# Kernel tuning notes

Hardware: AMD Instinct MI355X
Metric: run time of the kernel (lower is better)

Reference implementation:

```python
import jax, jax.numpy as jnp
import numpy as np

N = 6000      # nodes
E = 150000    # edges (avg degree ~25, close to _AVG_DEGREE=23.4)
K = 9         # (lmax+1)^2 spherical coefficients, lmax=2
C = 128       # sphere_channels
H = 8         # num_heads
V = 16        # attn_value_channels (H*V == C)
L = 2         # num_layers
B = 512       # num_distance_basis
RMAX = 5.0
EPS = 1e-6


def _rms_sh(x):
    # rms_norm_sh-style normalization over (coefficients, channels)
    return x * jax.lax.rsqrt(jnp.mean(x * x, axis=(-2, -1), keepdims=True) + EPS)


def _seg_softmax(logits, seg, n):
    # numerically-stable per-destination-node softmax over incoming edges
    m = jax.ops.segment_max(logits, seg, num_segments=n)
    ex = jnp.exp(logits - m[seg])
    s = jax.ops.segment_sum(ex, seg, num_segments=n)
    return ex / (s[seg] + 1e-9)


def setup_inputs() -> dict:
    key = jax.random.key(0)
    ks = jax.random.split(key, 24)
    s = 0.02
    inp = {
        # graph / features
        "atom_feats": jax.random.randint(ks[0], (N, 4), 0, 10),
        "bond_feats": jax.random.randint(ks[1], (E, 3), 0, 8),
        "edge_index": jax.random.randint(ks[2], (2, E), 0, N),
        "edge_distance": jax.random.uniform(ks[3], (E,), jnp.float32, 0.0, RMAX),
        # embeddings
        "atom_emb": jax.random.normal(ks[4], (4, 10, C), jnp.float32) * s,
        "bond_emb": jax.random.normal(ks[5], (3, 8, C), jnp.float32) * s,
        # distance-basis edge MLP (edge_channels_list = [512, 128, 128])
        "W_rbf1": jax.random.normal(ks[6], (B, C), jnp.float32) * s,
        "b_rbf1": jnp.zeros((C,), jnp.float32),
        "W_rbf2": jax.random.normal(ks[7], (C, C), jnp.float32) * s,
        "b_rbf2": jnp.zeros((C,), jnp.float32),
        # per-layer attention params (stacked over L)
        "Wa1": jax.random.normal(ks[8], (L, 3 * C, C), jnp.float32) * s,
        "Wa2": jax.random.normal(ks[9], (L, C, H), jnp.float32) * s,
        "Wv": jax.random.normal(ks[10], (L, C, H * V), jnp.float32) * s,
        "Wg": jax.random.normal(ks[11], (L, C, H), jnp.float32) * s,
        "Wo": jax.random.normal(ks[12], (L, H * V, C), jnp.float32) * s,
        # per-layer FFN params
        "Wf1": jax.random.normal(ks[13], (L, C, 512), jnp.float32) * s,
        "Wf2": jax.random.normal(ks[14], (L, 512, C), jnp.float32) * s,
    }
    return inp


def _forward(atom_feats, bond_feats, edge_index, edge_distance,
             atom_emb, bond_emb, W_rbf1, b_rbf1, W_rbf2, b_rbf2,
             Wa1, Wa2, Wv, Wg, Wo, Wf1, Wf2):
    src, dst = edge_index[0], edge_index[1]

    # --- atom embedding into l=0 coefficient of the SH node state ---
    a0 = sum(atom_emb[f][atom_feats[:, f]] for f in range(4))      # [N, C]
    x = jnp.zeros((N, K, C), a0.dtype).at[:, 0, :].set(a0)          # [N, K, C]

    # --- gaussian distance basis + edge embedding MLP + bond features ---
    centers = jnp.linspace(0.0, RMAX, B)
    width = RMAX / B
    rbf = jnp.exp(-((edge_distance[:, None] - centers[None, :]) / width) ** 2)  # [E, B]
    e = jax.nn.silu(rbf @ W_rbf1 + b_rbf1) @ W_rbf2 + b_rbf2                    # [E, C]
    e = e + sum(bond_emb[f][bond_feats[:, f]] for f in range(3))

    for l in range(L):
        # ---- SO(2)-style graph attention block ----
        xn = _rms_sh(x)
        xs = xn[src]                                                 # [E, K, C] gather
        inv = jnp.concatenate([xn[src, 0], xn[dst, 0], e], axis=-1)  # invariant feats [E, 3C]
        logits = jax.nn.silu(inv @ Wa1[l]) @ Wa2[l]                  # [E, H]
        alpha = _seg_softmax(logits, dst, N)                         # renormalized attention
        gate = jax.nn.sigmoid(e @ Wg[l])                             # edge-embedding gate [E, H]
        v = jnp.einsum('ekc,chv->ekhv', xs, Wv[l].reshape(C, H, V))  # [E, K, H, V]
        v = v * (alpha * gate)[:, None, :, None]
        msg = v.reshape(E, K, H * V)
        agg = jax.ops.segment_sum(msg, dst, num_segments=N)          # scatter [N, K, H*V]
        x = x + jnp.einsum('nkd,dc->nkc', agg, Wo[l])

        # ---- equivariant FFN with separable S2-style activation ----
        xn = _rms_sh(x)
        h = jnp.einsum('nkc,cf->nkf', xn, Wf1[l])                    # [N, K, 512]
        h0 = jax.nn.silu(h[:, :1, :])                                # l=0 scalar path
        hr = h[:, 1:, :] * jax.nn.sigmoid(h[:, :1, :])               # gated l>0 path
        h = jnp.concatenate([h0, hr], axis=1)
        x = x + jnp.einsum('nkf,fc->nkc', h, Wf2[l])

    return _rms_sh(x)


def reference(atom_feats, bond_feats, edge_index, edge_distance,
              atom_emb, bond_emb, W_rbf1, b_rbf1, W_rbf2, b_rbf2,
              Wa1, Wa2, Wv, Wg, Wo, Wf1, Wf2):
    return _forward(atom_feats, bond_feats, edge_index, edge_distance,
                    atom_emb, bond_emb, W_rbf1, b_rbf1, W_rbf2, b_rbf2,
                    Wa1, Wa2, Wv, Wg, Wo, Wf1, Wf2)
```

## Files before the change

kernel.cpp:

```cpp
#include <hip/hip_runtime.h>

#define NN 6000
#define NE 150000
#define TBM 2048
#define TROWS (TBM + 1)

typedef unsigned int uint;
typedef unsigned short ushort;
typedef __attribute__((ext_vector_type(8))) short short8v;
typedef __attribute__((ext_vector_type(4))) float float4v;

__device__ __forceinline__ float siluf(float x) { return x / (1.f + __expf(-x)); }
__device__ __forceinline__ float sigmf(float x) { return 1.f / (1.f + __expf(-x)); }
__device__ __forceinline__ uint pack2bf(float lo, float hi) {
    uint ul = __float_as_uint(lo);
    ul = (ul + 0x7fffu + ((ul >> 16) & 1u)) >> 16;
    uint uh = __float_as_uint(hi);
    uh = ((uh + 0x7fffu + ((uh >> 16) & 1u)) >> 16) << 16;
    return ul | uh;
}
__device__ __forceinline__ ushort f2bf(float f) {
    uint u = __float_as_uint(f);
    return (ushort)((u + 0x7fffu + ((u >> 16) & 1u)) >> 16);
}
__device__ __forceinline__ float2 up2(uint u) {
    return make_float2(__uint_as_float(u << 16), __uint_as_float(u & 0xffff0000u));
}

__global__ __launch_bounds__(256)
void k_prep(const float* __restrict__ W2, const float* __restrict__ b2,
            const float* __restrict__ Wa1, const float* __restrict__ Wg,
            const float* __restrict__ bemb,
            const float* __restrict__ Wf1, const float* __restrict__ Wf2,
            const float* __restrict__ Wv, const float* __restrict__ Wa2,
            const float* __restrict__ Wo,
            float* __restrict__ W2A, float* __restrict__ W2G,
            float* __restrict__ bA, float* __restrict__ bG,
            uint* __restrict__ BAcb, float* __restrict__ BGc,
            ushort* __restrict__ Wf1x, ushort* __restrict__ Wf2x,
            ushort* __restrict__ Wvx, ushort* __restrict__ Wa1sx,
            ushort* __restrict__ Wa1dx, ushort* __restrict__ Wa2x,
            ushort* __restrict__ Wox)
{
    __shared__ float w2_s[8][132];
    const int l = blockIdx.y, bx = blockIdx.x, tid = threadIdx.x;
    const float* Wa1e = Wa1 + (size_t)l * 384 * 128 + 256 * 128;
    const float* Wgl  = Wg  + (size_t)l * 128 * 8;

    if (bx < 16) {
        const int i0 = bx * 8;
        for (int q = tid; q < 8 * 32; q += 256) {
            int ni = q >> 5, j4 = (q & 31) * 4;
            *reinterpret_cast<float4*>(&w2_s[ni][j4]) =
                *reinterpret_cast<const float4*>(&W2[(size_t)(i0 + ni) * 128 + j4]);
        }
        __syncthreads();
        const int j = tid & 127, ng = tid >> 7;
        float a[4] = {0.f, 0.f, 0.f, 0.f};
        #pragma unroll 4
        for (int k4 = 0; k4 < 128; k4 += 4) {
            float w0 = Wa1e[(k4 + 0) * 128 + j];
            float w1 = Wa1e[(k4 + 1) * 128 + j];
            float w2v = Wa1e[(k4 + 2) * 128 + j];
            float w3 = Wa1e[(k4 + 3) * 128 + j];
            #pragma unroll
            for (int r = 0; r < 4; ++r) {
                const float4 xv = *reinterpret_cast<const float4*>(&w2_s[ng * 4 + r][k4]);
                a[r] += xv.x * w0 + xv.y * w1 + xv.z * w2v + xv.w * w3;
            }
        }
        #pragma unroll
        for (int r = 0; r < 4; ++r)
            W2A[(size_t)l * 16384 + (size_t)(i0 + ng * 4 + r) * 128 + j] = a[r];
    } else if (bx == 16) {
        const int i = tid & 127, hq = tid >> 7;
        float a[4] = {0.f, 0.f, 0.f, 0.f};
        for (int k = 0; k < 128; ++k) {
            float w = W2[(size_t)i * 128 + k];
            const float4 g4 = *reinterpret_cast<const float4*>(&Wgl[k * 8 + hq * 4]);
            a[0] += w * g4.x; a[1] += w * g4.y; a[2] += w * g4.z; a[3] += w * g4.w;
        }
        #pragma unroll
        for (int q = 0; q < 4; ++q)
            W2G[(size_t)l * 1024 + (size_t)i * 8 + hq * 4 + q] = a[q];
    } else if (bx == 17) {
        if (tid < 128) {
            float s = 0.f;
            for (int k = 0; k < 128; ++k) s += b2[k] * Wa1e[k * 128 + tid];
            bA[l * 128 + tid] = s;
        } else if (tid < 136) {
            int h = tid - 128;
            float s = 0.f;
            for (int k = 0; k < 128; ++k) s += b2[k] * Wgl[k * 8 + h];
            bG[l * 8 + h] = s;
        }
    } else if (bx < 274) {
        const int cb = (bx - 18) * 2 + (tid >> 7);
        const int c = tid & 127;
        const int b[3] = {cb >> 6, (cb >> 3) & 7, cb & 7};
        float s = 0.f;
        #pragma unroll
        for (int f = 0; f < 3; ++f) {
            const float* er = &bemb[(size_t)(f * 8 + b[f]) * 128];
            for (int k = 0; k < 128; ++k)
                s += er[k] * Wa1e[k * 128 + c];
        }
        float hi = __shfl_down(s, 1, 64);
        if ((c & 1) == 0)
            BAcb[(size_t)l * 512 * 64 + (size_t)cb * 64 + (c >> 1)] = pack2bf(s, hi);
        if (c < 8) {
            float g = 0.f;
            #pragma unroll
            for (int f = 0; f < 3; ++f) {
                const float* er = &bemb[(size_t)(f * 8 + b[f]) * 128];
                for (int k = 0; k < 128; ++k)
                    g += er[k] * Wgl[k * 8 + c];
            }
            BGc[(size_t)l * 512 * 8 + (size_t)cb * 8 + c] = g;
        }
    } else {
        const int sub = (bx - 274) * 4 + (tid >> 6);
        const int lane = tid & 63;
        if (sub < 128) {
            const int nt = sub >> 2, kt = sub & 3;
            const float* src = Wf1 + (size_t)l * 65536;
            ushort* dst = Wf1x + (size_t)l * 65536 + ((size_t)sub * 64 + lane) * 8;
            #pragma unroll
            for (int j = 0; j < 8; ++j)
                dst[j] = f2bf(src[(size_t)(kt * 32 + (lane >> 4) * 8 + j) * 512 + nt * 16 + (lane & 15)]);
        } else if (sub < 256) {
            const int b2x = sub - 128;
            const int nt = b2x >> 4, kt = b2x & 15;
            const float* src = Wf2 + (size_t)l * 65536;
            ushort* dst = Wf2x + (size_t)l * 65536 + ((size_t)b2x * 64 + lane) * 8;
            #pragma unroll
            for (int j = 0; j < 8; ++j)
                dst[j] = f2bf(src[(size_t)(kt * 32 + (lane >> 4) * 8 + j) * 128 + nt * 16 + (lane & 15)]);
        } else if (sub < 352) {
            const int b3 = sub - 256;
            const int mat = b3 >> 5, blk = b3 & 31;
            const int nt = blk >> 2, kt = blk & 3;
            const float* src;
            ushort* dst;
            if (mat == 0)      { src = Wv  + (size_t)l * 16384;             dst = Wvx   + (size_t)l * 16384; }
            else if (mat == 1) { src = Wa1 + (size_t)l * 384 * 128;         dst = Wa1sx + (size_t)l * 16384; }
            else               { src = Wa1 + (size_t)l * 384 * 128 + 16384; dst = Wa1dx + (size_t)l * 16384; }
            dst += ((size_t)blk * 64 + lane) * 8;
            #pragma unroll
            for (int j = 0; j < 8; ++j)
                dst[j] = f2bf(src[(size_t)(kt * 32 + (lane >> 4) * 8 + j) * 128 + nt * 16 + (lane & 15)]);
        } else if (sub < 356) {
            const int kt = sub - 352;
            const int col = lane & 15;
            const float* src = Wa2 + (size_t)l * 128 * 8;
            ushort* dst = Wa2x + (size_t)l * 2048 + ((size_t)kt * 64 + lane) * 8;
            #pragma unroll
            for (int j = 0; j < 8; ++j) {
                int krow = kt * 32 + (lane >> 4) * 8 + j;
                dst[j] = (col < 8) ? f2bf(src[(size_t)krow * 8 + col]) : (ushort)0;
            }
        } else {
            const int blk = sub - 356;
            const int nt = blk >> 2, kt = blk & 3;
            const float* src = Wo + (size_t)l * 16384;
            ushort* dst = Wox + (size_t)l * 16384 + ((size_t)blk * 64 + lane) * 8;
            #pragma unroll
            for (int j = 0; j < 8; ++j)
                dst[j] = f2bf(src[(size_t)(kt * 32 + (lane >> 4) * 8 + j) * 128 + nt * 16 + (lane & 15)]);
        }
    }
}

__device__ __forceinline__
void node_gemm3(const ushort a_s[16][136], int tid, int n0,
                const ushort* __restrict__ Wvx, const ushort* __restrict__ Wa1sx,
                const ushort* __restrict__ Wa1dx,
                uint* __restrict__ Vb, uint* __restrict__ Psb, uint* __restrict__ Pdb)
{
    const int l = tid & 63, wq = tid >> 6;
    const int lr = l & 15, lk = l >> 4;
    #pragma unroll
    for (int jb = 0; jb < 6; ++jb) {
        int job = wq * 6 + jb;
        int mat = job >> 3, nt = job & 7;
        const ushort* W = (mat == 0) ? Wvx : (mat == 1 ? Wa1sx : Wa1dx);
        uint* O = (mat == 0) ? Vb : (mat == 1 ? Psb : Pdb);
        float4v acc = (float4v){0.f, 0.f, 0.f, 0.f};
        #pragma unroll
        for (int ks = 0; ks < 4; ++ks) {
            short8v af = *reinterpret_cast<const short8v*>(&a_s[lr][lk * 8 + ks * 32]);
            short8v bf = *reinterpret_cast<const short8v*>(&W[((size_t)(nt * 4 + ks) * 64 + l) * 8]);
            acc = __builtin_amdgcn_mfma_f32_16x16x32_bf16(af, bf, acc, 0, 0, 0);
        }
        #pragma unroll
        for (int r = 0; r < 4; ++r) {
            float v = acc[r];
            float vn = __shfl_xor(v, 1, 64);
            if ((l & 1) == 0) {
                int row = lk * 4 + r, col = nt * 16 + lr;
                O[(size_t)(n0 + row) * 64 + (col >> 1)] = pack2bf(v, vn);
            }
        }
    }
}

__device__ __forceinline__
void node_gemm3_8w(const ushort a_s[16][136], int tid, int n0,
                   const ushort* __restrict__ Wvx, const ushort* __restrict__ Wa1sx,
                   const ushort* __restrict__ Wa1dx,
                   uint* __restrict__ Vb, uint* __restrict__ Psb, uint* __restrict__ Pdb)
{
    const int l = tid & 63, w = tid >> 6;
    const int lr = l & 15, lk = l >> 4;
    #pragma unroll
    for (int jb = 0; jb < 3; ++jb) {
        int job = w * 3 + jb;
        int mat = job >> 3, nt = job & 7;
        const ushort* W = (mat == 0) ? Wvx : (mat == 1 ? Wa1sx : Wa1dx);
        uint* O = (mat == 0) ? Vb : (mat == 1 ? Psb : Pdb);
        float4v acc = (float4v){0.f, 0.f, 0.f, 0.f};
        #pragma unroll
        for (int ks = 0; ks < 4; ++ks) {
            short8v af = *reinterpret_cast<const short8v*>(&a_s[lr][lk * 8 + ks * 32]);
            short8v bf = *reinterpret_cast<const short8v*>(&W[((size_t)(nt * 4 + ks) * 64 + l) * 8]);
            acc = __builtin_amdgcn_mfma_f32_16x16x32_bf16(af, bf, acc, 0, 0, 0);
        }
        #pragma unroll
        for (int r = 0; r < 4; ++r) {
            float v = acc[r];
            float vn = __shfl_xor(v, 1, 64);
            if ((l & 1) == 0) {
                int row = lk * 4 + r, col = nt * 16 + lr;
                O[(size_t)(n0 + row) * 64 + (col >> 1)] = pack2bf(v, vn);
            }
        }
    }
}

__global__ __launch_bounds__(256)
void k_prep2(const float* __restrict__ W1, const float* __restrict__ b1,
             const float* __restrict__ W2A, const float* __restrict__ W2G,
             const float* __restrict__ bA, const float* __restrict__ bG,
             uint* __restrict__ TAb, float* __restrict__ TG,
             const int* __restrict__ af, const float* __restrict__ aemb,
             float* __restrict__ x, int* __restrict__ deg,
             const ushort* __restrict__ Wvx, const ushort* __restrict__ Wa1sx,
             const ushort* __restrict__ Wa1dx,
             uint* __restrict__ Vb, uint* __restrict__ Psb, uint* __restrict__ Pdb)
{
    __shared__ float rbf_s[8][32];
    __shared__ int   bs_s[8];
    __shared__ float t1_s[8][132];
    __shared__ ushort a_s[16][136];
    const int tid = threadIdx.x, bx = blockIdx.x;

    if (bx < 514) {
        const int l = (bx >= 257) ? 1 : 0;
        const int r0 = (bx - l * 257) * 8;
        {
            int ri = tid >> 5, j = tid & 31;
            int row = min(r0 + ri, TBM);
            float d = (float)row * (5.0f / TBM);
            const float step = 5.0f / 511.0f;
            const float invw = 512.0f / 5.0f;
            int b0 = (int)(d * (511.0f / 5.0f) + 0.5f);
            int bs = min(max(b0 - 16, 0), 512 - 32);
            if (j == 0) bs_s[ri] = bs;
            float z = (d - (float)(bs + j) * step) * invw;
            rbf_s[ri][j] = __expf(-z * z);
        }
        __syncthreads();
        #pragma unroll
        for (int pass = 0; pass < 4; ++pass) {
            int idx = pass * 256 + tid;
            int ri = idx >> 7, c = idx & 127;
            int bs = bs_s[ri];
            float t = b1[c];
            #pragma unroll
            for (int j = 0; j < 32; ++j)
                t += rbf_s[ri][j] * W1[(bs + j) * 128 + c];
            t1_s[ri][c] = siluf(t);
        }
        __syncthreads();

        const float* W2Al = W2A + (size_t)l * 16384;
        const int c = tid & 127, ng = tid >> 7;
        float a[4];
        #pragma unroll
        for (int r = 0; r < 4; ++r) a[r] = bA[l * 128 + c];
        #pragma unroll 4
        for (int k4 = 0; k4 < 128; k4 += 4) {
            float w0 = W2Al[(k4 + 0) * 128 + c];
            float w1 = W2Al[(k4 + 1) * 128 + c];
            float w2v = W2Al[(k4 + 2) * 128 + c];
            float w3 = W2Al[(k4 + 3) * 128 + c];
            #pragma unroll
            for (int r = 0; r < 4; ++r) {
                const float4 xv = *reinterpret_cast<const float4*>(&t1_s[ng * 4 + r][k4]);
                a[r] += xv.x * w0 + xv.y * w1 + xv.z * w2v + xv.w * w3;
            }
        }
        #pragma unroll
        for (int r = 0; r < 4; ++r) {
            float hi = __shfl_down(a[r], 1, 64);
            int row = r0 + ng * 4 + r;
            if (((c & 1) == 0) && row <= TBM)
                TAb[(size_t)l * TROWS * 64 + (size_t)row * 64 + (c >> 1)] = pack2bf(a[r], hi);
        }
        if (tid < 64) {
            int ri = tid >> 3, h = tid & 7;
            int row = r0 + ri;
            if (row <= TBM) {
                const float* W2Gl = W2G + (size_t)l * 1024;
                float s = bG[l * 8 + h];
                #pragma unroll 8
                for (int k = 0; k < 128; ++k)
                    s += t1_s[ri][k] * W2Gl[k * 8 + h];
                TG[(size_t)l * TROWS * 8 + (size_t)row * 8 + h] = s;
            }
        }
    } else {
        const int n0 = (bx - 514) * 16;
        if (tid < 16) deg[n0 + tid] = 0;
        {
            int ni = tid >> 4, c8 = (tid & 15) * 8;
            int n = n0 + ni;
            float v[8];
            #pragma unroll
            for (int q = 0; q < 8; ++q) v[q] = 0.f;
            #pragma unroll
            for (int f = 0; f < 4; ++f) {
                int idx = af[n * 4 + f];
                const float* er = &aemb[(size_t)(f * 10 + idx) * 128 + c8];
                float4 e0 = *reinterpret_cast<const float4*>(er);
                float4 e1 = *reinterpret_cast<const float4*>(er + 4);
                v[0] += e0.x; v[1] += e0.y; v[2] += e0.z; v[3] += e0.w;
                v[4] += e1.x; v[5] += e1.y; v[6] += e1.z; v[7] += e1.w;
            }
            float* xr = &x[(size_t)n * 128 + c8];
            *reinterpret_cast<float4*>(xr)     = make_float4(v[0], v[1], v[2], v[3]);
            *reinterpret_cast<float4*>(xr + 4) = make_float4(v[4], v[5], v[6], v[7]);
            float ss = 0.f;
            #pragma unroll
            for (int q = 0; q < 8; ++q) ss += v[q] * v[q];
            #pragma unroll
            for (int m = 1; m < 16; m <<= 1) ss += __shfl_xor(ss, m, 16);
            float r = rsqrtf(ss * (1.0f / 1152.0f) + 1e-6f);
            uint4 pk;
            pk.x = pack2bf(v[0] * r, v[1] * r);
            pk.y = pack2bf(v[2] * r, v[3] * r);
            pk.z = pack2bf(v[4] * r, v[5] * r);
            pk.w = pack2bf(v[6] * r, v[7] * r);
            *reinterpret_cast<uint4*>(&a_s[ni][c8]) = pk;
        }
        __syncthreads();
        node_gemm3(a_s, tid, n0, Wvx, Wa1sx, Wa1dx, Vb, Psb, Pdb);
    }
}

__global__ __launch_bounds__(256)
void k_hist(const int* __restrict__ eidx, int* __restrict__ deg)
{
    int e = blockIdx.x * 256 + threadIdx.x;
    if (e < NE) atomicAdd(&deg[eidx[NE + e]], 1);
}

__global__ __launch_bounds__(1024)
void k_scan(const int* __restrict__ deg, int* __restrict__ off, int* __restrict__ cursor)
{
    __shared__ int part[1024];
    const int t = threadIdx.x;
    const int base = t * 6;
    int loc[6]; int s = 0;
    #pragma unroll
    for (int i = 0; i < 6; ++i) {
        int d = (base + i < NN) ? deg[base + i] : 0;
        loc[i] = s; s += d;
    }
    part[t] = s;
    __syncthreads();
    for (int o = 1; o < 1024; o <<= 1) {
        int v = (t >= o) ? part[t - o] : 0;
        __syncthreads();
        part[t] += v;
        __syncthreads();
    }
    int pre = (t > 0) ? part[t - 1] : 0;
    #pragma unroll
    for (int i = 0; i < 6; ++i) {
        if (base + i < NN) {
            int v = pre + loc[i];
            off[base + i] = v;
            cursor[base + i] = v;
        }
    }
    if (t == 1023) off[NN] = part[1023];
}

__global__ __launch_bounds__(256)
void k_fill(const int* __restrict__ eidx, const int* __restrict__ bondf,
            const float* __restrict__ dist, int* __restrict__ cursor,
            int* __restrict__ srcp, int4* __restrict__ erec)
{
    int e = blockIdx.x * 256 + threadIdx.x;
    if (e < NE) {
        int d = eidx[NE + e];
        int p = atomicAdd(&cursor[d], 1);
        int sn = eidx[e];
        srcp[p] = sn;
        erec[p] = make_int4(sn, d, __float_as_int(dist[e]),
                            bondf[e * 3 + 0] * 64 + bondf[e * 3 + 1] * 8 + bondf[e * 3 + 2]);
    }
}

__global__ __launch_bounds__(256)
void k_attn(const int4* __restrict__ erec,
            const uint* __restrict__ Psb, const uint* __restrict__ Pdb,
            const uint* __restrict__ TAbl, const float* __restrict__ TGl,
            const uint* __restrict__ BAcbl, const float* __restrict__ BGcl,
            const ushort* __restrict__ Wa2xl,
            float2* __restrict__ nex)
{
    __shared__ ushort t_s[32][136];
    __shared__ float gate_s[32][8];
    const int tid = threadIdx.x;
    const int p0 = blockIdx.x * 32;

    {
        const int ei = tid >> 3, g = tid & 7;
        const int p = min(p0 + ei, NE - 1);
        const int4 er = erec[p];
        const int sn = er.x, dn = er.y;
        const float d = __int_as_float(er.z);
        const int cb = er.w;
        float u = d * ((float)TBM / 5.0f);
        int i = min((int)u, TBM - 1);
        float f = u - (float)i, f1 = 1.f - f;

        uint ps[8], pd[8], t0[8], t1v[8], ba[8];
        {
            const uint4* pp = reinterpret_cast<const uint4*>(&Psb[(size_t)sn * 64 + g * 8]);
            uint4 a = pp[0], b = pp[1];
            ps[0]=a.x; ps[1]=a.y; ps[2]=a.z; ps[3]=a.w; ps[4]=b.x; ps[5]=b.y; ps[6]=b.z; ps[7]=b.w;
            pp = reinterpret_cast<const uint4*>(&Pdb[(size_t)dn * 64 + g * 8]);
            a = pp[0]; b = pp[1];
            pd[0]=a.x; pd[1]=a.y; pd[2]=a.z; pd[3]=a.w; pd[4]=b.x; pd[5]=b.y; pd[6]=b.z; pd[7]=b.w;
            pp = reinterpret_cast<const uint4*>(&TAbl[(size_t)i * 64 + g * 8]);
            a = pp[0]; b = pp[1];
            t0[0]=a.x; t0[1]=a.y; t0[2]=a.z; t0[3]=a.w; t0[4]=b.x; t0[5]=b.y; t0[6]=b.z; t0[7]=b.w;
            pp = reinterpret_cast<const uint4*>(&TAbl[(size_t)(i + 1) * 64 + g * 8]);
            a = pp[0]; b = pp[1];
            t1v[0]=a.x; t1v[1]=a.y; t1v[2]=a.z; t1v[3]=a.w; t1v[4]=b.x; t1v[5]=b.y; t1v[6]=b.z; t1v[7]=b.w;
            pp = reinterpret_cast<const uint4*>(&BAcbl[(size_t)cb * 64 + g * 8]);
            a = pp[0]; b = pp[1];
            ba[0]=a.x; ba[1]=a.y; ba[2]=a.z; ba[3]=a.w; ba[4]=b.x; ba[5]=b.y; ba[6]=b.z; ba[7]=b.w;
        }
        uint tw[8];
        #pragma unroll
        for (int q = 0; q < 8; ++q) {
            float2 vs = up2(ps[q]), vd = up2(pd[q]), v0 = up2(t0[q]), v1 = up2(t1v[q]), vb = up2(ba[q]);
            float s0 = siluf(vs.x + vd.x + f1 * v0.x + f * v1.x + vb.x);
            float s1 = siluf(vs.y + vd.y + f1 * v0.y + f * v1.y + vb.y);
            tw[q] = pack2bf(s0, s1);
        }
        uint4* tp = reinterpret_cast<uint4*>(&t_s[ei][g * 16]);
        tp[0] = make_uint4(tw[0], tw[1], tw[2], tw[3]);
        tp[1] = make_uint4(tw[4], tw[5], tw[6], tw[7]);
        if (g == 0) {
            const float4* tg0 = reinterpret_cast<const float4*>(&TGl[(size_t)i * 8]);
            const float4* bg4 = reinterpret_cast<const float4*>(&BGcl[(size_t)cb * 8]);
            #pragma unroll
            for (int q = 0; q < 2; ++q) {
                float4 g0 = tg0[q], g1 = tg0[q + 2], bb = bg4[q];
                gate_s[ei][4 * q + 0] = f1 * g0.x + f * g1.x + bb.x;
                gate_s[ei][4 * q + 1] = f1 * g0.y + f * g1.y + bb.y;
                gate_s[ei][4 * q + 2] = f1 * g0.z + f * g1.z + bb.z;
                gate_s[ei][4 * q + 3] = f1 * g0.w + f * g1.w + bb.w;
            }
        }
    }
    __syncthreads();

    {
        const int wq = tid >> 6, l = tid & 63;
        if (wq < 2) {
            const int lr = l & 15, lk = l >> 4;
            float4v acc = (float4v){0.f, 0.f, 0.f, 0.f};
            #pragma unroll
            for (int ks = 0; ks < 4; ++ks) {
                short8v af = *reinterpret_cast<const short8v*>(&t_s[wq * 16 + lr][lk * 8 + ks * 32]);
                short8v bf = *reinterpret_cast<const short8v*>(&Wa2xl[((size_t)ks * 64 + l) * 8]);
                acc = __builtin_amdgcn_mfma_f32_16x16x32_bf16(af, bf, acc, 0, 0, 0);
            }
            const int h = l & 15;
            if (h < 8) {
                #pragma unroll
                for (int r = 0; r < 4; ++r) {
                    int ei = wq * 16 + lk * 4 + r;
                    int p = p0 + ei;
                    if (p < NE) {
                        float ex = __expf(acc[r]);
                        nex[(size_t)p * 8 + h] = make_float2(ex * sigmf(gate_s[ei][h]), ex);
                    }
                }
            }
        }
    }
}

template<int LAST>
__global__ __launch_bounds__(512)
void k_layer_fused(float* __restrict__ x,
                   const int* __restrict__ off, const int* __restrict__ srcp,
                   const float2* __restrict__ nex, const uint* __restrict__ Vb,
                   const ushort* __restrict__ Woxl,
                   const ushort* __restrict__ Wf1xl, const ushort* __restrict__ Wf2xl,
                   float* __restrict__ out,
                   const ushort* __restrict__ WvxN, const ushort* __restrict__ Wa1sxN,
                   const ushort* __restrict__ Wa1dxN,
                   uint* __restrict__ VbO, uint* __restrict__ Psb, uint* __restrict__ Pdb)
{
    __shared__ ushort a_s[16][136];
    __shared__ ushort h_s[16][520];
    __shared__ float xf_s[16][132];
    const int tid = threadIdx.x;
    const int n0 = blockIdx.x * 16;
    const int ni = tid >> 5;
    const int ci = tid & 31;
    const int c4 = ci * 4;

    {
        *reinterpret_cast<float4*>(&xf_s[ni][c4]) =
            *reinterpret_cast<const float4*>(&x[(size_t)(n0 + ni) * 128 + c4]);
    }

    {
        const int n = n0 + ni;
        const int h = ci >> 2;
        const int cd2 = ci * 2;
        const int s = off[n], t = off[n + 1];
        float a0 = 0.f, a1 = 0.f, a2 = 0.f, a3 = 0.f, es = 0.f;
        int p = s;
        for (; p + 4 <= t; p += 4) {
            int sn0 = srcp[p + 0], sn1 = srcp[p + 1], sn2 = srcp[p + 2], sn3 = srcp[p + 3];
            float2 ne0 = nex[(size_t)(p + 0) * 8 + h];
            float2 ne1 = nex[(size_t)(p + 1) * 8 + h];
            float2 ne2 = nex[(size_t)(p + 2) * 8 + h];
            float2 ne3 = nex[(size_t)(p + 3) * 8 + h];
            uint2 u0 = *reinterpret_cast<const uint2*>(&Vb[(size_t)sn0 * 64 + cd2]);
            uint2 u1 = *reinterpret_cast<const uint2*>(&Vb[(size_t)sn1 * 64 + cd2]);
            uint2 u2 = *reinterpret_cast<const uint2*>(&Vb[(size_t)sn2 * 64 + cd2]);
            uint2 u3 = *reinterpret_cast<const uint2*>(&Vb[(size_t)sn3 * 64 + cd2]);
            es += ne0.y + ne1.y + ne2.y + ne3.y;
            float2 v;
            v = up2(u0.x); a0 += ne0.x * v.x; a1 += ne0.x * v.y;
            v = up2(u0.y); a2 += ne0.x * v.x; a3 += ne0.x * v.y;
            v = up2(u1.x); a0 += ne1.x * v.x; a1 += ne1.x * v.y;
            v = up2(u1.y); a2 += ne1.x * v.x; a3 += ne1.x * v.y;
            v = up2(u2.x); a0 += ne2.x * v.x; a1 += ne2.x * v.y;
            v = up2(u2.y); a2 += ne2.x * v.x; a3 += ne2.x * v.y;
            v = up2(u3.x); a0 += ne3.x * v.x; a1 += ne3.x * v.y;
            v = up2(u3.y); a2 += ne3.x * v.x; a3 += ne3.x * v.y;
        }
        for (; p < t; ++p) {
            int sn = srcp[p];
            float2 ne = nex[(size_t)p * 8 + h];
            uint2 u = *reinterpret_cast<const uint2*>(&Vb[(size_t)sn * 64 + cd2]);
            es += ne.y;
            float2 v;
            v = up2(u.x); a0 += ne.x * v.x; a1 += ne.x * v.y;
            v = up2(u.y); a2 += ne.x * v.x; a3 += ne.x * v.y;
        }
        float sinv = 1.f / (es + 1e-9f);
        uint2 pk;
        pk.x = pack2bf(a0 * sinv, a1 * sinv);
        pk.y = pack2bf(a2 * sinv, a3 * sinv);
        *reinterpret_cast<uint2*>(&a_s[ni][c4]) = pk;
    }
    __syncthreads();

    const int l  = tid & 63;
    const int w  = tid >> 6;
    const int lr = l & 15, lk = l >> 4;

    {
        float4v acc = (float4v){0.f, 0.f, 0.f, 0.f};
        #pragma unroll
        for (int ks = 0; ks < 4; ++ks) {
            short8v af = *reinterpret_cast<const short8v*>(&a_s[lr][lk * 8 + ks * 32]);
            short8v bf = *reinterpret_cast<const short8v*>(&Woxl[((size_t)(w * 4 + ks) * 64 + l) * 8]);
            acc = __builtin_amdgcn_mfma_f32_16x16x32_bf16(af, bf, acc, 0, 0, 0);
        }
        #pragma unroll
        for (int r = 0; r < 4; ++r)
            xf_s[lk * 4 + r][w * 16 + lr] += acc[r];
    }
    __syncthreads();

    {
        float4 v = *reinterpret_cast<const float4*>(&xf_s[ni][c4]);
        float ss = v.x * v.x + v.y * v.y + v.z * v.z + v.w * v.w;
        #pragma unroll
        for (int m = 1; m < 32; m <<= 1) ss += __shfl_xor(ss, m, 32);
        float r = rsqrtf(ss * (1.0f / 1152.0f) + 1e-6f);
        uint2 pk;
        pk.x = pack2bf(v.x * r, v.y * r);
        pk.y = pack2bf(v.z * r, v.w * r);
        *reinterpret_cast<uint2*>(&a_s[ni][c4]) = pk;
    }
    __syncthreads();

    {
        float4v acc[4];
        #pragma unroll
        for (int nf = 0; nf < 4; ++nf) acc[nf] = (float4v){0.f, 0.f, 0.f, 0.f};
        #pragma unroll
        for (int ks = 0; ks < 4; ++ks) {
            short8v af = *reinterpret_cast<const short8v*>(&a_s[lr][lk * 8 + ks * 32]);
            #pragma unroll
            for (int nf = 0; nf < 4; ++nf) {
                int nt = w * 4 + nf;
                short8v bf = *reinterpret_cast<const short8v*>(&Wf1xl[((size_t)(nt * 4 + ks) * 64 + l) * 8]);
                acc[nf] = __builtin_amdgcn_mfma_f32_16x16x32_bf16(af, bf, acc[nf], 0, 0, 0);
            }
        }
        #pragma unroll
        for (int nf = 0; nf < 4; ++nf) {
            #pragma unroll
            for (int r = 0; r < 4; ++r) {
                float v = siluf(acc[nf][r]);
                float vn = __shfl_xor(v, 1, 64);
                if ((l & 1) == 0) {
                    int row = lk * 4 + r;
                    int col = (w * 4 + nf) * 16 + lr;
                    *reinterpret_cast<uint*>(&h_s[row][col]) = pack2bf(v, vn);
                }
            }
        }
    }
    __syncthreads();

    {
        float4v acc = (float4v){0.f, 0.f, 0.f, 0.f};
        #pragma unroll 4
        for (int ks = 0; ks < 16; ++ks) {
            short8v af = *reinterpret_cast<const short8v*>(&h_s[lr][lk * 8 + ks * 32]);
            short8v bf = *reinterpret_cast<const short8v*>(&Wf2xl[((size_t)(w * 16 + ks) * 64 + l) * 8]);
            acc = __builtin_amdgcn_mfma_f32_16x16x32_bf16(af, bf, acc, 0, 0, 0);
        }
        #pragma unroll
        for (int r = 0; r < 4; ++r)
            xf_s[lk * 4 + r][w * 16 + lr] += acc[r];
    }
    __syncthreads();

    {
        float4 v = *reinterpret_cast<const float4*>(&xf_s[ni][c4]);
        float ss = v.x * v.x + v.y * v.y + v.z * v.z + v.w * v.w;
        #pragma unroll
        for (int m = 1; m < 32; m <<= 1) ss += __shfl_xor(ss, m, 32);
        float r = rsqrtf(ss * (1.0f / 1152.0f) + 1e-6f);

        if (!LAST) {
            *reinterpret_cast<float4*>(&x[(size_t)(n0 + ni) * 128 + c4]) = v;
            uint2 pk;
            pk.x = pack2bf(v.x * r, v.y * r);
            pk.y = pack2bf(v.z * r, v.w * r);
            *reinterpret_cast<uint2*>(&a_s[ni][c4]) = pk;
            __syncthreads();
            node_gemm3_8w(a_s, tid, n0, WvxN, Wa1sxN, Wa1dxN, VbO, Psb, Pdb);
        } else {
            size_t base = (size_t)(n0 + ni) * 1152 + c4;
            *reinterpret_cast<float4*>(&out[base]) = make_float4(v.x * r, v.y * r, v.z * r, v.w * r);
            const float4 z4 = make_float4(0.f, 0.f, 0.f, 0.f);
            #pragma unroll
            for (int k = 1; k < 9; ++k)
                *reinterpret_cast<float4*>(&out[base + (size_t)k * 128]) = z4;
        }
    }
}

extern "C" void kernel_launch(void* const* d_in, const int* in_sizes, int n_in,
                              void* d_out, int out_size, void* d_ws, size_t ws_size,
                              hipStream_t stream)
{
    const int*   atom_feats = (const int*)d_in[0];
    const int*   bond_feats = (const int*)d_in[1];
    const int*   edge_index = (const int*)d_in[2];
    const float* edge_dist  = (const float*)d_in[3];
    const float* atom_emb   = (const float*)d_in[4];
    const float* bond_emb   = (const float*)d_in[5];
    const float* W_rbf1     = (const float*)d_in[6];
    const float* b_rbf1     = (const float*)d_in[7];
    const float* W_rbf2     = (const float*)d_in[8];
    const float* b_rbf2     = (const float*)d_in[9];
    const float* Wa1        = (const float*)d_in[10];
    const float* Wa2        = (const float*)d_in[11];
    const float* Wv         = (const float*)d_in[12];
    const float* Wg         = (const float*)d_in[13];
    const float* Wo         = (const float*)d_in[14];
    const float* Wf1        = (const float*)d_in[15];
    const float* Wf2        = (const float*)d_in[16];
    float* out = (float*)d_out;

    float* ws   = (float*)d_ws;
    float* x    = ws;
    float2* nex = (float2*)(x + NN * 128);
    float* W2A  = (float*)(nex + (size_t)NE * 8);
    float* W2G  = W2A  + 2 * 16384;
    float* bA   = W2G  + 2 * 1024;
    float* bG   = bA   + 2 * 128;
    float* TG   = bG   + 16;
    float* BGc  = TG   + 2 * (size_t)TROWS * 8;
    uint* Vb    = (uint*)(BGc + 2 * 512 * 8);
    uint* Psb   = Vb  + NN * 64;
    uint* Pdb   = Psb + NN * 64;
    uint* TAb   = Pdb + NN * 64;
    uint* BAcb  = TAb + 2 * (size_t)TROWS * 64;
    ushort* Wf1x  = (ushort*)(BAcb + 2 * 512 * 64);
    ushort* Wf2x  = Wf1x  + 2 * 65536;
    ushort* Wvx   = Wf2x  + 2 * 65536;
    ushort* Wa1sx = Wvx   + 2 * 16384;
    ushort* Wa1dx = Wa1sx + 2 * 16384;
    ushort* Wa2x  = Wa1dx + 2 * 16384;
    ushort* Wox   = Wa2x  + 2 * 2048;
    int* deg    = (int*)(Wox + 2 * 16384);
    int* off    = deg + NN;
    int* cursor = off + NN + 1;
    int* srcp   = cursor + NN;
    int4* erec  = (int4*)(srcp + NE);

    k_prep<<<dim3(371, 2), 256, 0, stream>>>(W_rbf2, b_rbf2, Wa1, Wg, bond_emb,
        Wf1, Wf2, Wv, Wa2, Wo, W2A, W2G, bA, bG, BAcb, BGc,
        Wf1x, Wf2x, Wvx, Wa1sx, Wa1dx, Wa2x, Wox);
    k_prep2<<<514 + NN / 16, 256, 0, stream>>>(W_rbf1, b_rbf1, W2A, W2G, bA, bG, TAb, TG,
        atom_feats, atom_emb, x, deg, Wvx, Wa1sx, Wa1dx, Vb, Psb, Pdb);

    k_hist<<<(NE + 255) / 256, 256, 0, stream>>>(edge_index, deg);
    k_scan<<<1, 1024, 0, stream>>>(deg, off, cursor);
    k_fill<<<(NE + 255) / 256, 256, 0, stream>>>(edge_index, bond_feats, edge_dist,
                                                 cursor, srcp, erec);

    for (int l = 0; l < 2; ++l) {
        k_attn<<<(NE + 31) / 32, 256, 0, stream>>>(erec,
            Psb, Pdb,
            TAb + (size_t)l * TROWS * 64, TG + (size_t)l * TROWS * 8,
            BAcb + (size_t)l * 512 * 64, BGc + (size_t)l * 512 * 8,
            Wa2x + (size_t)l * 2048, nex);
        if (l == 0)
            k_layer_fused<0><<<NN / 16, 512, 0, stream>>>(x, off, srcp, nex, Vb,
                Wox, Wf1x, Wf2x, out,
                Wvx + 16384, Wa1sx + 16384, Wa1dx + 16384, Vb, Psb, Pdb);
        else
            k_layer_fused<1><<<NN / 16, 512, 0, stream>>>(x, off, srcp, nex, Vb,
                Wox + 16384, Wf1x + 65536, Wf2x + 65536, out,
                Wvx, Wa1sx, Wa1dx, Vb, Psb, Pdb);
    }
}
```

Baseline: 155.4 us.

## Fuse histogram into prep2, pack edge softmax terms to bf16, widen attn tiles

Moves the degree zeroing into k_prep and the degree histogram into extra blocks of k_prep2, which removes one kernel launch. The per-edge (gated exp, exp) pair is now stored as two bf16 values in one uint instead of a float2, halving that buffer's traffic in k_attn and k_layer_fused at the cost of precision in the softmax numerator and denominator. k_attn now handles 64 edges per block so all four wavefronts run the MFMA logit step instead of two. The histogram blocks depend on the zeroing done in the earlier k_prep launch on the same stream, which keeps the order correct.

```diff
diff --git a/kernel.cpp b/kernel.cpp
--- a/kernel.cpp
+++ b/kernel.cpp
@@ -40,7 +40,7 @@
             ushort* __restrict__ Wf1x, ushort* __restrict__ Wf2x,
             ushort* __restrict__ Wvx, ushort* __restrict__ Wa1sx,
             ushort* __restrict__ Wa1dx, ushort* __restrict__ Wa2x,
-            ushort* __restrict__ Wox)
+            ushort* __restrict__ Wox, int* __restrict__ deg)
 {
     __shared__ float w2_s[8][132];
     const int l = blockIdx.y, bx = blockIdx.x, tid = threadIdx.x;
@@ -93,6 +93,8 @@
             float s = 0.f;
             for (int k = 0; k < 128; ++k) s += b2[k] * Wgl[k * 8 + h];
             bG[l * 8 + h] = s;
+        } else if (l == 0) {
+            for (int i = tid - 136; i < NN; i += 120) if (i >= 0) deg[i] = 0;
         }
     } else if (bx < 274) {
         const int cb = (bx - 18) * 2 + (tid >> 7);
@@ -244,6 +246,7 @@
              uint* __restrict__ TAb, float* __restrict__ TG,
              const int* __restrict__ af, const float* __restrict__ aemb,
              float* __restrict__ x, int* __restrict__ deg,
+             const int* __restrict__ eidx,
              const ushort* __restrict__ Wvx, const ushort* __restrict__ Wa1sx,
              const ushort* __restrict__ Wa1dx,
              uint* __restrict__ Vb, uint* __restrict__ Psb, uint* __restrict__ Pdb)
@@ -319,9 +322,8 @@
                 TG[(size_t)l * TROWS * 8 + (size_t)row * 8 + h] = s;
             }
         }
-    } else {
+    } else if (bx < 889) {
         const int n0 = (bx - 514) * 16;
-        if (tid < 16) deg[n0 + tid] = 0;
         {
             int ni = tid >> 4, c8 = (tid & 15) * 8;
             int n = n0 + ni;
@@ -355,14 +357,10 @@
         }
         __syncthreads();
         node_gemm3(a_s, tid, n0, Wvx, Wa1sx, Wa1dx, Vb, Psb, Pdb);
-    }
-}
-
-__global__ __launch_bounds__(256)
-void k_hist(const int* __restrict__ eidx, int* __restrict__ deg)
-{
-    int e = blockIdx.x * 256 + threadIdx.x;
-    if (e < NE) atomicAdd(&deg[eidx[NE + e]], 1);
+    } else {
+        int e = (bx - 889) * 256 + tid;
+        if (e < NE) atomicAdd(&deg[eidx[NE + e]], 1);
+    }
 }
 
 __global__ __launch_bounds__(1024)
@@ -419,15 +417,17 @@
             const uint* __restrict__ TAbl, const float* __restrict__ TGl,
             const uint* __restrict__ BAcbl, const float* __restrict__ BGcl,
             const ushort* __restrict__ Wa2xl,
-            float2* __restrict__ nex)
-{
-    __shared__ ushort t_s[32][136];
-    __shared__ float gate_s[32][8];
+            uint* __restrict__ nexp)
+{
+    __shared__ ushort t_s[64][136];
+    __shared__ float gate_s[64][8];
     const int tid = threadIdx.x;
-    const int p0 = blockIdx.x * 32;
-
-    {
-        const int ei = tid >> 3, g = tid & 7;
+    const int p0 = blockIdx.x * 64;
+
+    #pragma unroll
+    for (int half = 0; half < 2; ++half) {
+        const int ei = (tid >> 3) + half * 32;
+        const int g = tid & 7;
         const int p = min(p0 + ei, NE - 1);
         const int4 er = erec[p];
         const int sn = er.x, dn = er.y;
@@ -483,25 +483,23 @@
 
     {
         const int wq = tid >> 6, l = tid & 63;
-        if (wq < 2) {
-            const int lr = l & 15, lk = l >> 4;
-            float4v acc = (float4v){0.f, 0.f, 0.f, 0.f};
-            #pragma unroll
-            for (int ks = 0; ks < 4; ++ks) {
-                short8v af = *reinterpret_cast<const short8v*>(&t_s[wq * 16 + lr][lk * 8 + ks * 32]);
-                short8v bf = *reinterpret_cast<const short8v*>(&Wa2xl[((size_t)ks * 64 + l) * 8]);
-                acc = __builtin_amdgcn_mfma_f32_16x16x32_bf16(af, bf, acc, 0, 0, 0);
-            }
-            const int h = l & 15;
-            if (h < 8) {
-                #pragma unroll
-                for (int r = 0; r < 4; ++r) {
-                    int ei = wq * 16 + lk * 4 + r;
-                    int p = p0 + ei;
-                    if (p < NE) {
-                        float ex = __expf(acc[r]);
-                        nex[(size_t)p * 8 + h] = make_float2(ex * sigmf(gate_s[ei][h]), ex);
-                    }
+        const int lr = l & 15, lk = l >> 4;
+        float4v acc = (float4v){0.f, 0.f, 0.f, 0.f};
+        #pragma unroll
+        for (int ks = 0; ks < 4; ++ks) {
+            short8v af = *reinterpret_cast<const short8v*>(&t_s[wq * 16 + lr][lk * 8 + ks * 32]);
+            short8v bf = *reinterpret_cast<const short8v*>(&Wa2xl[((size_t)ks * 64 + l) * 8]);
+            acc = __builtin_amdgcn_mfma_f32_16x16x32_bf16(af, bf, acc, 0, 0, 0);
+        }
+        const int h = l & 15;
+        if (h < 8) {
+            #pragma unroll
+            for (int r = 0; r < 4; ++r) {
+                int ei = wq * 16 + lk * 4 + r;
+                int p = p0 + ei;
+                if (p < NE) {
+                    float ex = __expf(acc[r]);
+                    nexp[(size_t)p * 8 + h] = pack2bf(ex * sigmf(gate_s[ei][h]), ex);
                 }
             }
         }
@@ -512,7 +510,7 @@
 __global__ __launch_bounds__(512)
 void k_layer_fused(float* __restrict__ x,
                    const int* __restrict__ off, const int* __restrict__ srcp,
-                   const float2* __restrict__ nex, const uint* __restrict__ Vb,
+                   const uint* __restrict__ nexp, const uint* __restrict__ Vb,
                    const ushort* __restrict__ Woxl,
                    const ushort* __restrict__ Wf1xl, const ushort* __restrict__ Wf2xl,
                    float* __restrict__ out,
@@ -543,10 +541,10 @@
         int p = s;
         for (; p + 4 <= t; p += 4) {
             int sn0 = srcp[p + 0], sn1 = srcp[p + 1], sn2 = srcp[p + 2], sn3 = srcp[p + 3];
-            float2 ne0 = nex[(size_t)(p + 0) * 8 + h];
-            float2 ne1 = nex[(size_t)(p + 1) * 8 + h];
-            float2 ne2 = nex[(size_t)(p + 2) * 8 + h];
-            float2 ne3 = nex[(size_t)(p + 3) * 8 + h];
+            float2 ne0 = up2(nexp[(size_t)(p + 0) * 8 + h]);
+            float2 ne1 = up2(nexp[(size_t)(p + 1) * 8 + h]);
+            float2 ne2 = up2(nexp[(size_t)(p + 2) * 8 + h]);
+            float2 ne3 = up2(nexp[(size_t)(p + 3) * 8 + h]);
             uint2 u0 = *reinterpret_cast<const uint2*>(&Vb[(size_t)sn0 * 64 + cd2]);
             uint2 u1 = *reinterpret_cast<const uint2*>(&Vb[(size_t)sn1 * 64 + cd2]);
             uint2 u2 = *reinterpret_cast<const uint2*>(&Vb[(size_t)sn2 * 64 + cd2]);
@@ -564,7 +562,7 @@
         }
         for (; p < t; ++p) {
             int sn = srcp[p];
-            float2 ne = nex[(size_t)p * 8 + h];
+            float2 ne = up2(nexp[(size_t)p * 8 + h]);
             uint2 u = *reinterpret_cast<const uint2*>(&Vb[(size_t)sn * 64 + cd2]);
             es += ne.y;
             float2 v;
@@ -705,8 +703,8 @@
 
     float* ws   = (float*)d_ws;
     float* x    = ws;
-    float2* nex = (float2*)(x + NN * 128);
-    float* W2A  = (float*)(nex + (size_t)NE * 8);
+    uint* nexp  = (uint*)(x + NN * 128);
+    float* W2A  = (float*)(nexp + (size_t)NE * 8);
     float* W2G  = W2A  + 2 * 16384;
     float* bA   = W2G  + 2 * 1024;
     float* bG   = bA   + 2 * 128;
@@ -732,27 +730,27 @@
 
     k_prep<<<dim3(371, 2), 256, 0, stream>>>(W_rbf2, b_rbf2, Wa1, Wg, bond_emb,
         Wf1, Wf2, Wv, Wa2, Wo, W2A, W2G, bA, bG, BAcb, BGc,
-        Wf1x, Wf2x, Wvx, Wa1sx, Wa1dx, Wa2x, Wox);
-    k_prep2<<<514 + NN / 16, 256, 0, stream>>>(W_rbf1, b_rbf1, W2A, W2G, bA, bG, TAb, TG,
-        atom_feats, atom_emb, x, deg, Wvx, Wa1sx, Wa1dx, Vb, Psb, Pdb);
-
-    k_hist<<<(NE + 255) / 256, 256, 0, stream>>>(edge_index, deg);
+        Wf1x, Wf2x, Wvx, Wa1sx, Wa1dx, Wa2x, Wox, deg);
+    k_prep2<<<889 + (NE + 255) / 256, 256, 0, stream>>>(W_rbf1, b_rbf1, W2A, W2G, bA, bG,
+        TAb, TG, atom_feats, atom_emb, x, deg, edge_index,
+        Wvx, Wa1sx, Wa1dx, Vb, Psb, Pdb);
+
     k_scan<<<1, 1024, 0, stream>>>(deg, off, cursor);
     k_fill<<<(NE + 255) / 256, 256, 0, stream>>>(edge_index, bond_feats, edge_dist,
                                                  cursor, srcp, erec);
 
     for (int l = 0; l < 2; ++l) {
-        k_attn<<<(NE + 31) / 32, 256, 0, stream>>>(erec,
+        k_attn<<<(NE + 63) / 64, 256, 0, stream>>>(erec,
             Psb, Pdb,
             TAb + (size_t)l * TROWS * 64, TG + (size_t)l * TROWS * 8,
             BAcb + (size_t)l * 512 * 64, BGc + (size_t)l * 512 * 8,
-            Wa2x + (size_t)l * 2048, nex);
+            Wa2x + (size_t)l * 2048, nexp);
         if (l == 0)
-            k_layer_fused<0><<<NN / 16, 512, 0, stream>>>(x, off, srcp, nex, Vb,
+            k_layer_fused<0><<<NN / 16, 512, 0, stream>>>(x, off, srcp, nexp, Vb,
                 Wox, Wf1x, Wf2x, out,
                 Wvx + 16384, Wa1sx + 16384, Wa1dx + 16384, Vb, Psb, Pdb);
         else
-            k_layer_fused<1><<<NN / 16, 512, 0, stream>>>(x, off, srcp, nex, Vb,
+            k_layer_fused<1><<<NN / 16, 512, 0, stream>>>(x, off, srcp, nexp, Vb,
                 Wox + 16384, Wf1x + 65536, Wf2x + 65536, out,
                 Wvx, Wa1sx, Wa1dx, Vb, Psb, Pdb);
     }
```

After: 149.6 us, median of 2. 1.04x faster.
